# Optimization experiments

Measured on AMD Instinct MI355X. Metric: run time of the kernel, lower is better.

Reference implementation:

```python
import jax, jax.numpy as jnp
import numpy as np

N_NODES = 100000
N_EDGES = 1600000
NUM_GRAPHS = 1024
D_IN = 128
D_HID = 128
D_OUT = 2
LN_EPS = 1e-5


def setup_inputs() -> dict:
    key = jax.random.key(0)
    ks = jax.random.split(key, 10)
    x = jax.random.normal(ks[0], (N_NODES, D_IN), dtype=jnp.float32)
    edge_index = jax.random.randint(ks[1], (2, N_EDGES), 0, N_NODES, dtype=jnp.int64)
    batch = jnp.sort(jax.random.randint(ks[2], (N_NODES,), 0, NUM_GRAPHS, dtype=jnp.int64))
    s = 0.05  # weight scale to keep activations sane
    return {
        "x": x,
        "edge_index": edge_index,
        "batch": batch,
        "W1l": jax.random.normal(ks[3], (D_HID, D_IN), dtype=jnp.float32) * s,
        "b1l": jnp.zeros((D_HID,), dtype=jnp.float32),
        "W1r": jax.random.normal(ks[4], (D_HID, D_IN), dtype=jnp.float32) * s,
        "W2l": jax.random.normal(ks[5], (D_HID, D_HID), dtype=jnp.float32) * s,
        "b2l": jnp.zeros((D_HID,), dtype=jnp.float32),
        "W2r": jax.random.normal(ks[6], (D_HID, D_HID), dtype=jnp.float32) * s,
        "ln_g": jnp.ones((D_HID,), dtype=jnp.float32),
        "ln_b": jnp.zeros((D_HID,), dtype=jnp.float32),
        "Wlin": jax.random.normal(ks[7], (D_OUT, D_HID), dtype=jnp.float32) * s,
        "blin": jnp.zeros((D_OUT,), dtype=jnp.float32),
    }


def _sage_conv(x, src, dst, Wl, bl, Wr):
    # PyG SAGEConv with mean aggregation: lin_l(mean_{j in N(i)} x_j) + lin_r(x_i)
    msg_sum = jax.ops.segment_sum(x[src], dst, num_segments=N_NODES)
    deg = jax.ops.segment_sum(jnp.ones((src.shape[0], 1), x.dtype), dst, num_segments=N_NODES)
    agg = msg_sum / jnp.maximum(deg, 1.0)  # isolated nodes -> 0
    return agg @ Wl.T + bl + x @ Wr.T  # lin_r has no bias (PyG default)


def reference(x, edge_index, batch, W1l, b1l, W1r, W2l, b2l, W2r, ln_g, ln_b, Wlin, blin):
    src, dst = edge_index[0], edge_index[1]
    h = jax.nn.relu(_sage_conv(x, src, dst, W1l, b1l, W1r))
    h = jax.nn.relu(_sage_conv(h, src, dst, W2l, b2l, W2r))
    # global_add_pool over graphs
    g = jax.ops.segment_sum(h, batch, num_segments=NUM_GRAPHS)  # [G, D_HID]
    # LayerNorm over last dim
    mu = jnp.mean(g, axis=-1, keepdims=True)
    var = jnp.var(g, axis=-1, keepdims=True)
    gn = (g - mu) * jax.lax.rsqrt(var + LN_EPS) * ln_g + ln_b
    return gn @ Wlin.T + blin  # [G, D_OUT]
```

## Files before the change

kernel.cpp:

```cpp
#include <hip/hip_runtime.h>
#include <hip/hip_bf16.h>

#define N_NODES   100000
#define N_EDGES   1600000
#define NUM_GRAPHS 1024
#define D         128
#define LN_EPS    1e-5f
#define NBUCKETS  196
#define CAP       9216
#define CHUNK     4096

typedef __attribute__((ext_vector_type(8))) short short8;
typedef __attribute__((ext_vector_type(4))) float floatx4;
typedef __attribute__((ext_vector_type(2))) float f32x2;

static __device__ __forceinline__ float bf2f(unsigned int u) {
    return __uint_as_float(u << 16);
}
static __device__ __forceinline__ unsigned short f2bf(float f) {
    __hip_bfloat16 h = __float2bfloat16(f);
    return *reinterpret_cast<unsigned short*>(&h);
}
static __device__ __forceinline__ void acc4(f32x2* acc, uint4 v) {
    acc[0] += (f32x2){__uint_as_float(v.x << 16), __uint_as_float(v.x & 0xffff0000u)};
    acc[1] += (f32x2){__uint_as_float(v.y << 16), __uint_as_float(v.y & 0xffff0000u)};
    acc[2] += (f32x2){__uint_as_float(v.z << 16), __uint_as_float(v.z & 0xffff0000u)};
    acc[3] += (f32x2){__uint_as_float(v.w << 16), __uint_as_float(v.w & 0xffff0000u)};
}

__global__ __launch_bounds__(256)
void prep_kernel(const float* __restrict__ x, unsigned short* __restrict__ xbf,
                 const float* __restrict__ W1l, const float* __restrict__ W1r,
                 const float* __restrict__ W2l, const float* __restrict__ W2r,
                 unsigned short* __restrict__ Wc1, unsigned short* __restrict__ Wc2,
                 int* __restrict__ cursor) {
    int i = blockIdx.x * 256 + threadIdx.x;
    float4 v = reinterpret_cast<const float4*>(x)[i];
    ushort4 o;
    o.x = f2bf(v.x); o.y = f2bf(v.y); o.z = f2bf(v.z); o.w = f2bf(v.w);
    reinterpret_cast<ushort4*>(xbf)[i] = o;
    if (blockIdx.x < 256) {
        int layer = i >> 15;
        int rem = i & 32767;
        int c = rem >> 8;
        int k = rem & 255;
        const float* Wl = layer ? W2l : W1l;
        const float* Wr = layer ? W2r : W1r;
        unsigned short* dst = layer ? Wc2 : Wc1;
        float wv = (k < 128) ? Wl[c * 128 + k] : Wr[c * 128 + (k - 128)];
        dst[c * 256 + k] = f2bf(wv);
    }
    if (blockIdx.x == 256 && threadIdx.x < NBUCKETS)
        cursor[threadIdx.x] = threadIdx.x * CAP;
}

__global__ __launch_bounds__(256)
void bin_scatter_kernel(const int* __restrict__ src, const int* __restrict__ dst,
                        int* __restrict__ cursor, uint2* __restrict__ binned) {
    __shared__ int cnt[NBUCKETS];
    __shared__ int base[NBUCKETS];
    int chunkBase = blockIdx.x * CHUNK;
    for (int i = threadIdx.x; i < NBUCKETS; i += 256) cnt[i] = 0;
    __syncthreads();
    int es[16], ed[16], lofs[16];
    #pragma unroll
    for (int j = 0; j < 16; ++j) {
        int e = chunkBase + j * 256 + threadIdx.x;
        if (e < N_EDGES) {
            es[j] = src[e];
            ed[j] = dst[e];
            lofs[j] = atomicAdd(&cnt[ed[j] >> 9], 1);
        }
    }
    __syncthreads();
    for (int i = threadIdx.x; i < NBUCKETS; i += 256) {
        int c = cnt[i];
        base[i] = c ? atomicAdd(&cursor[i], c) : 0;
    }
    __syncthreads();
    #pragma unroll
    for (int j = 0; j < 16; ++j) {
        int e = chunkBase + j * 256 + threadIdx.x;
        if (e < N_EDGES) {
            int b = ed[j] >> 9;
            int pos = base[b] + lofs[j];
            if (pos < (b + 1) * CAP)
                binned[pos] = make_uint2((unsigned)es[j], (unsigned)ed[j]);
        }
    }
}

__global__ __launch_bounds__(512)
void bucket_build_kernel(const uint2* __restrict__ binned, const int* __restrict__ cursor,
                         int2* __restrict__ row_info, int* __restrict__ src_sorted) {
    __shared__ int scnt[512];
    __shared__ int sscan[512];
    int b = blockIdx.x;
    int t = threadIdx.x;
    int lo = b * CAP;
    int hi = cursor[b];
    scnt[t] = 0;
    __syncthreads();
    for (int e = lo + t; e < hi; e += 512)
        atomicAdd(&scnt[binned[e].y & 511], 1);
    __syncthreads();
    int v = scnt[t];
    sscan[t] = v;
    __syncthreads();
    for (int off = 1; off < 512; off <<= 1) {
        int a = (t >= off) ? sscan[t - off] : 0;
        __syncthreads();
        sscan[t] += a;
        __syncthreads();
    }
    int ex = sscan[t] - v;
    int node = b * 512 + t;
    if (node < N_NODES) row_info[node] = make_int2(lo + ex, v);
    scnt[t] = ex;
    __syncthreads();
    for (int e = lo + t; e < hi; e += 512) {
        uint2 r = binned[e];
        int p = atomicAdd(&scnt[r.y & 511], 1);
        src_sorted[lo + p] = (int)r.x;
    }
}

__global__ __launch_bounds__(256)
void aggregate_kernel(const unsigned short* __restrict__ feat,
                      const int* __restrict__ src_sorted,
                      const int2* __restrict__ row_info,
                      unsigned short* __restrict__ aggout) {
    int wave = threadIdx.x >> 6;
    int lane = threadIdx.x & 63;
    int node = blockIdx.x * 4 + wave;
    int sub = lane >> 4;
    int ch = (lane & 15) * 8;
    int2 ri = row_info[node];
    int s = ri.x, deg = ri.y;
    const unsigned short* fb = feat + ch;
    f32x2 acc[4];
    acc[0] = acc[1] = acc[2] = acc[3] = (f32x2){0.f, 0.f};

    if (deg <= 64) {
        int si = 0;
        if (lane < deg) si = src_sorted[s + lane];
        int rounds = (deg + 3) >> 2;
        for (int r = 0; r < rounds; ++r) {
            int eidx = r * 4 + sub;
            int u = __shfl(si, eidx, 64);
            if (eidx < deg) {
                uint4 v = *(const uint4*)(fb + (size_t)u * 128);
                acc4(acc, v);
            }
        }
    } else {
        for (int j = s + sub; j < s + deg; j += 4) {
            int u = src_sorted[j];
            uint4 v = *(const uint4*)(fb + (size_t)u * 128);
            acc4(acc, v);
        }
    }
    #pragma unroll
    for (int i = 0; i < 4; ++i) {
        acc[i].x += __shfl_xor(acc[i].x, 16, 64);
        acc[i].y += __shfl_xor(acc[i].y, 16, 64);
        acc[i].x += __shfl_xor(acc[i].x, 32, 64);
        acc[i].y += __shfl_xor(acc[i].y, 32, 64);
    }
    float inv = 1.f / (float)(deg > 1 ? deg : 1);
    if (sub == 0) {
        uint4 ov;
        ov.x = (unsigned)f2bf(acc[0].x * inv) | ((unsigned)f2bf(acc[0].y * inv) << 16);
        ov.y = (unsigned)f2bf(acc[1].x * inv) | ((unsigned)f2bf(acc[1].y * inv) << 16);
        ov.z = (unsigned)f2bf(acc[2].x * inv) | ((unsigned)f2bf(acc[2].y * inv) << 16);
        ov.w = (unsigned)f2bf(acc[3].x * inv) | ((unsigned)f2bf(acc[3].y * inv) << 16);
        *(uint4*)(aggout + (size_t)node * 128 + ch) = ov;
    }
}

__global__ __launch_bounds__(256)
void gemm_kernel(const unsigned short* __restrict__ A1,
                 const unsigned short* __restrict__ A2,
                 const unsigned short* __restrict__ Wcat,
                 const float* __restrict__ bias,
                 unsigned short* __restrict__ out) {
    __shared__ unsigned short Asm[64][32];
    __shared__ unsigned short Wsm[128][32];
    int tid = threadIdx.x;
    int wave = tid >> 6;
    int lane = tid & 63;
    int nodeBase = blockIdx.x * 64;
    floatx4 acc[4][2];
    #pragma unroll
    for (int a = 0; a < 4; ++a)
        #pragma unroll
        for (int b = 0; b < 2; ++b) acc[a][b] = (floatx4){0.f, 0.f, 0.f, 0.f};

    int r = tid >> 2, sg = tid & 3;
    int quad = lane >> 4, m = lane & 15;

    for (int kc = 0; kc < 8; ++kc) {
        const unsigned short* Asrc = (kc < 4) ? A1 : A2;
        int kOff = (kc & 3) * 32;
        int node = nodeBase + r;
        float4 av = make_float4(0.f, 0.f, 0.f, 0.f);
        if (node < N_NODES) av = *(const float4*)(Asrc + (size_t)node * 128 + kOff + sg * 8);
        *(float4*)(&Asm[r][sg * 8]) = av;
        #pragma unroll
        for (int it = 0; it < 2; ++it) {
            int idx = tid + it * 256;
            int wr = idx >> 2, wsg = idx & 3;
            *(float4*)(&Wsm[wr][wsg * 8]) = *(const float4*)(Wcat + wr * 256 + kc * 32 + wsg * 8);
        }
        __syncthreads();
        short8 afr[4], bfr[2];
        #pragma unroll
        for (int nb = 0; nb < 4; ++nb)
            afr[nb] = *(const short8*)(&Asm[nb * 16 + m][quad * 8]);
        #pragma unroll
        for (int cb = 0; cb < 2; ++cb)
            bfr[cb] = *(const short8*)(&Wsm[wave * 32 + cb * 16 + m][quad * 8]);
        #pragma unroll
        for (int nb = 0; nb < 4; ++nb)
            #pragma unroll
            for (int cb = 0; cb < 2; ++cb)
                acc[nb][cb] = __builtin_amdgcn_mfma_f32_16x16x32_bf16(afr[nb], bfr[cb], acc[nb][cb], 0, 0, 0);
        __syncthreads();
    }
    #pragma unroll
    for (int cb = 0; cb < 2; ++cb) {
        int col = wave * 32 + cb * 16 + m;
        float bv = bias[col];
        #pragma unroll
        for (int nb = 0; nb < 4; ++nb) {
            #pragma unroll
            for (int rr = 0; rr < 4; ++rr) {
                int row = nodeBase + nb * 16 + quad * 4 + rr;
                if (row < N_NODES) {
                    float v = acc[nb][cb][rr] + bv;
                    v = v > 0.f ? v : 0.f;
                    out[(size_t)row * 128 + col] = f2bf(v);
                }
            }
        }
    }
}

__global__ __launch_bounds__(256)
void pool_ln_out_kernel(const unsigned short* __restrict__ h2,
                        const int* __restrict__ batch,
                        const float* __restrict__ ln_g, const float* __restrict__ ln_b,
                        const float* __restrict__ Wlin, const float* __restrict__ blin,
                        float* __restrict__ out) {
    int g = blockIdx.x;
    int t = threadIdx.x;
    int lane = t & 63, w = t >> 6;
    __shared__ int se[2];
    if (t < 2) {
        int target = g + t;
        int lo = 0, hi = N_NODES;
        while (lo < hi) {
            int mid = (lo + hi) >> 1;
            if (batch[mid] < target) lo = mid + 1; else hi = mid;
        }
        se[t] = lo;
    }
    __syncthreads();
    int s = se[0], e = se[1];
    int ns = t >> 4;
    int chg = t & 15;
    f32x2 a[4];
    a[0] = a[1] = a[2] = a[3] = (f32x2){0.f, 0.f};
    for (int n = s + ns; n < e; n += 16) {
        uint4 v = *(const uint4*)(h2 + (size_t)n * 128 + chg * 8);
        acc4(a, v);
    }
    #pragma unroll
    for (int i = 0; i < 4; ++i) {
        a[i].x += __shfl_xor(a[i].x, 16, 64);
        a[i].y += __shfl_xor(a[i].y, 16, 64);
        a[i].x += __shfl_xor(a[i].x, 32, 64);
        a[i].y += __shfl_xor(a[i].y, 32, 64);
    }
    __shared__ float sw[4][128];
    if (lane < 16) {
        #pragma unroll
        for (int k = 0; k < 4; ++k) {
            sw[w][chg * 8 + 2 * k]     = a[k].x;
            sw[w][chg * 8 + 2 * k + 1] = a[k].y;
        }
    }
    __syncthreads();
    __shared__ float red[128];
    float sum = 0.f;
    if (t < 128) {
        sum = sw[0][t] + sw[1][t] + sw[2][t] + sw[3][t];
        red[t] = sum;
    }
    __syncthreads();
    for (int off = 64; off > 0; off >>= 1) {
        if (t < off) red[t] += red[t + off];
        __syncthreads();
    }
    float mu = red[0] * (1.f / 128.f);
    __syncthreads();
    float dv = sum - mu;
    if (t < 128) red[t] = dv * dv;
    __syncthreads();
    for (int off = 64; off > 0; off >>= 1) {
        if (t < off) red[t] += red[t + off];
        __syncthreads();
    }
    float var = red[0] * (1.f / 128.f);
    __syncthreads();
    __shared__ float r0[128], r1[128];
    if (t < 128) {
        float gn = dv * rsqrtf(var + LN_EPS) * ln_g[t] + ln_b[t];
        r0[t] = gn * Wlin[t];
        r1[t] = gn * Wlin[128 + t];
    }
    __syncthreads();
    for (int off = 64; off > 0; off >>= 1) {
        if (t < off) { r0[t] += r0[t + off]; r1[t] += r1[t + off]; }
        __syncthreads();
    }
    if (t == 0) {
        out[g * 2 + 0] = r0[0] + blin[0];
        out[g * 2 + 1] = r1[0] + blin[1];
    }
}

extern "C" void kernel_launch(void* const* d_in, const int* in_sizes, int n_in,
                              void* d_out, int out_size, void* d_ws, size_t ws_size,
                              hipStream_t stream) {
    const float* x    = (const float*)d_in[0];
    const int*   ei   = (const int*)d_in[1];
    const int*   batch= (const int*)d_in[2];
    const float* W1l  = (const float*)d_in[3];
    const float* b1l  = (const float*)d_in[4];
    const float* W1r  = (const float*)d_in[5];
    const float* W2l  = (const float*)d_in[6];
    const float* b2l  = (const float*)d_in[7];
    const float* W2r  = (const float*)d_in[8];
    const float* ln_g = (const float*)d_in[9];
    const float* ln_b = (const float*)d_in[10];
    const float* Wlin = (const float*)d_in[11];
    const float* blin = (const float*)d_in[12];
    float* out = (float*)d_out;

    char* ws = (char*)d_ws;
    size_t off = 0;
    auto alloc = [&](size_t bytes) {
        char* p = ws + off;
        off = (off + bytes + 255) & ~(size_t)255;
        return p;
    };
    unsigned short* xbf  = (unsigned short*)alloc((size_t)N_NODES * D * 2);
    unsigned short* aggb = (unsigned short*)alloc((size_t)N_NODES * D * 2);
    unsigned short* h1   = (unsigned short*)alloc((size_t)N_NODES * D * 2);
    unsigned short* Wc1  = (unsigned short*)alloc(128 * 256 * 2);
    unsigned short* Wc2  = (unsigned short*)alloc(128 * 256 * 2);
    int2* row_info   = (int2*)alloc((size_t)N_NODES * 8);
    int* src_sorted  = (int*)alloc((size_t)NBUCKETS * CAP * 4);
    int* cursor      = (int*)alloc(NBUCKETS * 4);
    uint2* binned = (uint2*)aggb;

    const int* srcI = ei;
    const int* dstI = ei + N_EDGES;

    prep_kernel<<<12500, 256, 0, stream>>>(x, xbf, W1l, W1r, W2l, W2r, Wc1, Wc2, cursor);
    bin_scatter_kernel<<<(N_EDGES + CHUNK - 1) / CHUNK, 256, 0, stream>>>(srcI, dstI, cursor, binned);
    bucket_build_kernel<<<NBUCKETS, 512, 0, stream>>>(binned, cursor, row_info, src_sorted);

    aggregate_kernel<<<25000, 256, 0, stream>>>(xbf, src_sorted, row_info, aggb);
    gemm_kernel<<<1563, 256, 0, stream>>>(aggb, xbf, Wc1, b1l, h1);
    aggregate_kernel<<<25000, 256, 0, stream>>>(h1, src_sorted, row_info, aggb);
    gemm_kernel<<<1563, 256, 0, stream>>>(aggb, h1, Wc2, b2l, xbf);
    pool_ln_out_kernel<<<NUM_GRAPHS, 256, 0, stream>>>(xbf, batch, ln_g, ln_b, Wlin, blin, out);
}
```

Baseline: 329.3 us.

## Halve edge bucket width and keep GEMM weights in registers

Edge buckets now cover 256 destination nodes instead of 512, so there are twice as many buckets. This gives bucket_build more blocks of 256 threads and smaller shared scans. bucket_build also clamps the end of each bucket to its capacity. The GEMM kernel drops shared-memory staging and barriers: each wave preloads its full weight slice into registers and reads A fragments straight from global memory. This trades LDS traffic and syncs for more register pressure and uncoalesced direct loads.

```diff
diff --git a/kernel.cpp b/kernel.cpp
--- a/kernel.cpp
+++ b/kernel.cpp
@@ -6,8 +6,8 @@
 #define NUM_GRAPHS 1024
 #define D         128
 #define LN_EPS    1e-5f
-#define NBUCKETS  196
-#define CAP       9216
+#define NBUCKETS  391
+#define CAP       4864
 #define CHUNK     4096
 
 typedef __attribute__((ext_vector_type(8))) short short8;
@@ -50,8 +50,10 @@
         float wv = (k < 128) ? Wl[c * 128 + k] : Wr[c * 128 + (k - 128)];
         dst[c * 256 + k] = f2bf(wv);
     }
-    if (blockIdx.x == 256 && threadIdx.x < NBUCKETS)
-        cursor[threadIdx.x] = threadIdx.x * CAP;
+    if (blockIdx.x == 256) {
+        for (int b = threadIdx.x; b < NBUCKETS; b += 256)
+            cursor[b] = b * CAP;
+    }
 }
 
 __global__ __launch_bounds__(256)
@@ -69,7 +71,7 @@
         if (e < N_EDGES) {
             es[j] = src[e];
             ed[j] = dst[e];
-            lofs[j] = atomicAdd(&cnt[ed[j] >> 9], 1);
+            lofs[j] = atomicAdd(&cnt[ed[j] >> 8], 1);
         }
     }
     __syncthreads();
@@ -82,7 +84,7 @@
     for (int j = 0; j < 16; ++j) {
         int e = chunkBase + j * 256 + threadIdx.x;
         if (e < N_EDGES) {
-            int b = ed[j] >> 9;
+            int b = ed[j] >> 8;
             int pos = base[b] + lofs[j];
             if (pos < (b + 1) * CAP)
                 binned[pos] = make_uint2((unsigned)es[j], (unsigned)ed[j]);
@@ -90,37 +92,39 @@
     }
 }
 
-__global__ __launch_bounds__(512)
+__global__ __launch_bounds__(256)
 void bucket_build_kernel(const uint2* __restrict__ binned, const int* __restrict__ cursor,
                          int2* __restrict__ row_info, int* __restrict__ src_sorted) {
-    __shared__ int scnt[512];
-    __shared__ int sscan[512];
+    __shared__ int scnt[256];
+    __shared__ int sscan[256];
     int b = blockIdx.x;
     int t = threadIdx.x;
     int lo = b * CAP;
     int hi = cursor[b];
+    int cap_end = lo + CAP;
+    if (hi > cap_end) hi = cap_end;
     scnt[t] = 0;
     __syncthreads();
-    for (int e = lo + t; e < hi; e += 512)
-        atomicAdd(&scnt[binned[e].y & 511], 1);
+    for (int e = lo + t; e < hi; e += 256)
+        atomicAdd(&scnt[binned[e].y & 255], 1);
     __syncthreads();
     int v = scnt[t];
     sscan[t] = v;
     __syncthreads();
-    for (int off = 1; off < 512; off <<= 1) {
+    for (int off = 1; off < 256; off <<= 1) {
         int a = (t >= off) ? sscan[t - off] : 0;
         __syncthreads();
         sscan[t] += a;
         __syncthreads();
     }
     int ex = sscan[t] - v;
-    int node = b * 512 + t;
+    int node = b * 256 + t;
     if (node < N_NODES) row_info[node] = make_int2(lo + ex, v);
     scnt[t] = ex;
     __syncthreads();
-    for (int e = lo + t; e < hi; e += 512) {
+    for (int e = lo + t; e < hi; e += 256) {
         uint2 r = binned[e];
-        int p = atomicAdd(&scnt[r.y & 511], 1);
+        int p = atomicAdd(&scnt[r.y & 255], 1);
         src_sorted[lo + p] = (int)r.x;
     }
 }
@@ -184,48 +188,42 @@
                  const unsigned short* __restrict__ Wcat,
                  const float* __restrict__ bias,
                  unsigned short* __restrict__ out) {
-    __shared__ unsigned short Asm[64][32];
-    __shared__ unsigned short Wsm[128][32];
     int tid = threadIdx.x;
     int wave = tid >> 6;
     int lane = tid & 63;
+    int quad = lane >> 4, m = lane & 15;
     int nodeBase = blockIdx.x * 64;
+
+    short8 bfr[8][2];
+    #pragma unroll
+    for (int kc = 0; kc < 8; ++kc)
+        #pragma unroll
+        for (int cb = 0; cb < 2; ++cb)
+            bfr[kc][cb] = *(const short8*)(Wcat + (size_t)(wave * 32 + cb * 16 + m) * 256 + kc * 32 + quad * 8);
+
     floatx4 acc[4][2];
     #pragma unroll
     for (int a = 0; a < 4; ++a)
         #pragma unroll
         for (int b = 0; b < 2; ++b) acc[a][b] = (floatx4){0.f, 0.f, 0.f, 0.f};
 
-    int r = tid >> 2, sg = tid & 3;
-    int quad = lane >> 4, m = lane & 15;
-
+    #pragma unroll
     for (int kc = 0; kc < 8; ++kc) {
         const unsigned short* Asrc = (kc < 4) ? A1 : A2;
-        int kOff = (kc & 3) * 32;
-        int node = nodeBase + r;
-        float4 av = make_float4(0.f, 0.f, 0.f, 0.f);
-        if (node < N_NODES) av = *(const float4*)(Asrc + (size_t)node * 128 + kOff + sg * 8);
-        *(float4*)(&Asm[r][sg * 8]) = av;
-        #pragma unroll
-        for (int it = 0; it < 2; ++it) {
-            int idx = tid + it * 256;
-            int wr = idx >> 2, wsg = idx & 3;
-            *(float4*)(&Wsm[wr][wsg * 8]) = *(const float4*)(Wcat + wr * 256 + kc * 32 + wsg * 8);
-        }
-        __syncthreads();
-        short8 afr[4], bfr[2];
-        #pragma unroll
-        for (int nb = 0; nb < 4; ++nb)
-            afr[nb] = *(const short8*)(&Asm[nb * 16 + m][quad * 8]);
-        #pragma unroll
-        for (int cb = 0; cb < 2; ++cb)
-            bfr[cb] = *(const short8*)(&Wsm[wave * 32 + cb * 16 + m][quad * 8]);
+        int kOff = (kc & 3) * 32 + quad * 8;
+        short8 afr[4];
+        #pragma unroll
+        for (int nb = 0; nb < 4; ++nb) {
+            int row = nodeBase + nb * 16 + m;
+            afr[nb] = (row < N_NODES)
+                ? *(const short8*)(Asrc + (size_t)row * 128 + kOff)
+                : (short8){0, 0, 0, 0, 0, 0, 0, 0};
+        }
         #pragma unroll
         for (int nb = 0; nb < 4; ++nb)
             #pragma unroll
             for (int cb = 0; cb < 2; ++cb)
-                acc[nb][cb] = __builtin_amdgcn_mfma_f32_16x16x32_bf16(afr[nb], bfr[cb], acc[nb][cb], 0, 0, 0);
-        __syncthreads();
+                acc[nb][cb] = __builtin_amdgcn_mfma_f32_16x16x32_bf16(afr[nb], bfr[kc][cb], acc[nb][cb], 0, 0, 0);
     }
     #pragma unroll
     for (int cb = 0; cb < 2; ++cb) {
@@ -370,7 +368,7 @@
 
     prep_kernel<<<12500, 256, 0, stream>>>(x, xbf, W1l, W1r, W2l, W2r, Wc1, Wc2, cursor);
     bin_scatter_kernel<<<(N_EDGES + CHUNK - 1) / CHUNK, 256, 0, stream>>>(srcI, dstI, cursor, binned);
-    bucket_build_kernel<<<NBUCKETS, 512, 0, stream>>>(binned, cursor, row_info, src_sorted);
+    bucket_build_kernel<<<NBUCKETS, 256, 0, stream>>>(binned, cursor, row_info, src_sorted);
 
     aggregate_kernel<<<25000, 256, 0, stream>>>(xbf, src_sorted, row_info, aggb);
     gemm_kernel<<<1563, 256, 0, stream>>>(aggb, xbf, Wc1, b1l, h1);
```

Result: slower. 381.3 us (+15.8%).
